# Performance work log

Measured on AMD Instinct MI355X. Metric: run time of the kernel, lower is better.

## Reference

```python
import jax, jax.numpy as jnp
import numpy as np

DIM = 2048
N_EXPERTS = 64
TOP_K = 8
BIAS_UPDATE_RATE = 0.01
EPS = 1e-8


def setup_inputs() -> dict:
    key = jax.random.key(0)
    k_x, k_w = jax.random.split(key)
    x = jax.random.normal(k_x, (4, 8192, DIM), dtype=jnp.float32)
    gate_weight = jax.random.normal(k_w, (N_EXPERTS, DIM), dtype=jnp.float32) * 0.02
    adaptive_bias = jnp.zeros((N_EXPERTS,), dtype=jnp.float32)
    expert_usage = jnp.zeros((N_EXPERTS,), dtype=jnp.float32)
    return {"x": x, "gate_weight": gate_weight, "adaptive_bias": adaptive_bias,
            "expert_usage": expert_usage}


def reference(x, gate_weight, adaptive_bias, expert_usage):
    B, S, D = x.shape
    xf = x.reshape(-1, D)                                   # [T, D]
    scores = jnp.einsum('td,ed->te', xf, gate_weight)       # [T, E]
    scores = scores + adaptive_bias[None, :]
    probs = jax.nn.softmax(scores, axis=-1)
    top_w, top_idx = jax.lax.top_k(probs, TOP_K)            # [T, K]
    top_w = top_w / (jnp.sum(top_w, axis=-1, keepdims=True) + EPS)
    # training-mode adaptive-bias update (no-grad histogram of selected experts)
    usage = jnp.bincount(top_idx.reshape(-1), length=N_EXPERTS).astype(jnp.float32)
    usage = usage / (B * S * TOP_K)
    usage_diff = usage - 1.0 / N_EXPERTS
    new_adaptive_bias = adaptive_bias - BIAS_UPDATE_RATE * usage_diff
    new_expert_usage = 0.9 * expert_usage + 0.1 * usage
    top_w = top_w.reshape(B, S, TOP_K)
    top_idx = top_idx.reshape(B, S, TOP_K)
    return top_w, top_idx, new_adaptive_bias, new_expert_usage
```

## Files before the change

### kernel.cpp

```cpp
#include <hip/hip_runtime.h>
#include <math.h>

constexpr int DIM    = 2048;
constexpr int NEXP   = 64;
constexpr int TOPK   = 8;
constexpr int T_TOT  = 32768;

constexpr int TTILE  = 64;
constexpr int BK     = 64;
constexpr int NSTEP  = DIM / BK;

constexpr float GAP_TH = 5.0e-4f;

constexpr size_t OFF_W   = 0;
constexpr size_t OFF_IDX = (size_t)T_TOT * TOPK;
constexpr size_t OFF_B   = OFF_IDX * 2;
constexpr size_t OFF_U   = OFF_B + NEXP;


#define MAC(i, j, A, B) \
    acc[i][j] = fmaf(A.x, B.x, acc[i][j]); \
    acc[i][j] = fmaf(A.y, B.y, acc[i][j]); \
    acc[i][j] = fmaf(A.z, B.z, acc[i][j]); \
    acc[i][j] = fmaf(A.w, B.w, acc[i][j]);

__global__ __launch_bounds__(256, 4)
void moe_gate_main(const float* __restrict__ x,
                   const float* __restrict__ gw,
                   const float* __restrict__ bias,
                   float* __restrict__ out,
                   unsigned int* __restrict__ ws,
                   const unsigned int cap)
{
    __shared__ __align__(16) char smem[32768];
    __shared__ unsigned int hist[NEXP];

    const int tid = threadIdx.x;
    const int t0  = blockIdx.x * TTILE;

    if (tid < NEXP) hist[tid] = 0;

    const int r0  = tid >> 4;
    const int c   = tid & 15;
    const float* xb0 = x  + (size_t)(t0 + r0) * DIM + 4 * c;
    const float* wb0 = gw + (size_t)r0        * DIM + 4 * c;
    const int ls0 = r0 * 256 + ((c ^ (r0 & 7)) << 4);

    char* const Wt = smem;
    char* const Xt = smem + 16384;

    float acc[4][4];
    #pragma unroll
    for (int i = 0; i < 4; ++i)
        #pragma unroll
        for (int j = 0; j < 4; ++j) acc[i][j] = 0.0f;

    const int eg = tid & 15;
    const int tg = tid >> 4;
    const int wx = (eg & 7) << 4;
    const int tx = (tg & 7) << 4;

    for (int step = 0; step < NSTEP; ++step) {
        const int ko = step * BK;
        const float4 xv0 = *(const float4*)(xb0 + ko);
        const float4 xv1 = *(const float4*)(xb0 + ko + 16 * DIM);
        const float4 xv2 = *(const float4*)(xb0 + ko + 32 * DIM);
        const float4 xv3 = *(const float4*)(xb0 + ko + 48 * DIM);
        const float4 wv0 = *(const float4*)(wb0 + ko);
        const float4 wv1 = *(const float4*)(wb0 + ko + 16 * DIM);
        const float4 wv2 = *(const float4*)(wb0 + ko + 32 * DIM);
        const float4 wv3 = *(const float4*)(wb0 + ko + 48 * DIM);
        __syncthreads();
        *(float4*)(Xt + ls0)         = xv0;
        *(float4*)(Xt + ls0 + 4096)  = xv1;
        *(float4*)(Xt + ls0 + 8192)  = xv2;
        *(float4*)(Xt + ls0 + 12288) = xv3;
        *(float4*)(Wt + ls0)         = wv0;
        *(float4*)(Wt + ls0 + 4096)  = wv1;
        *(float4*)(Wt + ls0 + 8192)  = wv2;
        *(float4*)(Wt + ls0 + 12288) = wv3;
        __syncthreads();

        const char* wb = Wt + eg * 256;
        const char* xb = Xt + tg * 256;
        #pragma unroll
        for (int q = 0; q < 16; ++q) {
            const int wq = (q << 4) ^ wx;
            const int xq = (q << 4) ^ tx;
            const float4 a0 = *(const float4*)(wb + wq);
            const float4 a1 = *(const float4*)(wb + 4096  + wq);
            const float4 a2 = *(const float4*)(wb + 8192  + wq);
            const float4 a3 = *(const float4*)(wb + 12288 + wq);
            const float4 b0 = *(const float4*)(xb + xq);
            const float4 b1 = *(const float4*)(xb + 4096  + xq);
            const float4 b2 = *(const float4*)(xb + 8192  + xq);
            const float4 b3 = *(const float4*)(xb + 12288 + xq);
            MAC(0,0,a0,b0) MAC(0,1,a0,b1) MAC(0,2,a0,b2) MAC(0,3,a0,b3)
            MAC(1,0,a1,b0) MAC(1,1,a1,b1) MAC(1,2,a1,b2) MAC(1,3,a1,b3)
            MAC(2,0,a2,b0) MAC(2,1,a2,b1) MAC(2,2,a2,b2) MAC(2,3,a2,b3)
            MAC(3,0,a3,b0) MAC(3,1,a3,b1) MAC(3,2,a3,b2) MAC(3,3,a3,b3)
        }
    }

    __syncthreads();
    float* S = (float*)smem;
    #pragma unroll
    for (int i = 0; i < 4; ++i) {
        const int e = eg + 16 * i;
        const float b = bias[e];
        #pragma unroll
        for (int j = 0; j < 4; ++j)
            S[e * 65 + tg + 16 * j] = acc[i][j] + b;
    }
    __syncthreads();

    if (tid < TTILE) {
        const int t = tid;
        float bv[9]; int bi[9];
        #pragma unroll
        for (int j = 0; j < 9; ++j) { bv[j] = -INFINITY; bi[j] = 0; }
        for (int e = 0; e < NEXP; ++e) {
            const float v = S[e * 65 + t];
            if (v > bv[8]) {
                bv[8] = v; bi[8] = e;
                #pragma unroll
                for (int j = 8; j > 0; --j) {
                    if (bv[j] > bv[j - 1]) {
                        const float tv = bv[j]; bv[j] = bv[j-1]; bv[j-1] = tv;
                        const int   ti = bi[j]; bi[j] = bi[j-1]; bi[j-1] = ti;
                    }
                }
            }
        }
        float ming = bv[0] - bv[1];
        #pragma unroll
        for (int j = 1; j < 8; ++j) ming = fminf(ming, bv[j] - bv[j + 1]);
        bool amb = (ming < GAP_TH);

        if (amb) {
            const unsigned slot = atomicAdd(ws + NEXP, 1u);
            if (slot < cap) ws[NEXP + 1 + slot] = (unsigned)(t0 + t);
            else            amb = false;
        }

        const float m = bv[0];
        float Z = 0.0f;
        for (int e = 0; e < NEXP; ++e) Z += expf(S[e * 65 + t] - m);
        const float rZ = 1.0f / Z;
        float p[TOPK]; float wsum = 0.0f;
        #pragma unroll
        for (int j = 0; j < TOPK; ++j) { p[j] = expf(bv[j] - m) * rZ; wsum += p[j]; }
        const float rd = 1.0f / (wsum + 1e-8f);

        const size_t tglob = (size_t)(t0 + t);
        float4 w0 = { p[0]*rd, p[1]*rd, p[2]*rd, p[3]*rd };
        float4 w1 = { p[4]*rd, p[5]*rd, p[6]*rd, p[7]*rd };
        *(float4*)(out + OFF_W + tglob * TOPK)     = w0;
        *(float4*)(out + OFF_W + tglob * TOPK + 4) = w1;
        float4 i0 = { (float)bi[0], (float)bi[1], (float)bi[2], (float)bi[3] };
        float4 i1 = { (float)bi[4], (float)bi[5], (float)bi[6], (float)bi[7] };
        *(float4*)(out + OFF_IDX + tglob * TOPK)     = i0;
        *(float4*)(out + OFF_IDX + tglob * TOPK + 4) = i1;

        if (!amb) {
            #pragma unroll
            for (int j = 0; j < TOPK; ++j) atomicAdd(&hist[bi[j]], 1u);
        }
    }

    __syncthreads();
    if (tid < NEXP) atomicAdd(ws + tid, hist[tid]);
}

__global__ __launch_bounds__(256)
void moe_gate_refine(const float* __restrict__ x,
                     const float* __restrict__ gw,
                     const float* __restrict__ bias,
                     float* __restrict__ out,
                     unsigned int* __restrict__ ws,
                     const unsigned int cap)
{
    __shared__ __align__(16) float xs[DIM];
    __shared__ float S[NEXP];
    const unsigned nf = ws[NEXP];
    const unsigned nflag = nf < cap ? nf : cap;
    const unsigned* list = ws + NEXP + 1;

    for (unsigned ii = blockIdx.x; ii < nflag; ii += gridDim.x) {
        const size_t t = (size_t)list[ii];
        __syncthreads();
        #pragma unroll
        for (int jj = 0; jj < 2; ++jj) {
            const int f = threadIdx.x + jj * 256;
            ((float4*)xs)[f] = ((const float4*)(x + t * DIM))[f];
        }
        __syncthreads();

        const int e = threadIdx.x >> 2;
        const int q = threadIdx.x & 3;
        const float* wr = gw + (size_t)e * DIM + q * 512;
        const float* xr = xs + q * 512;
        double s = 0.0;
        for (int k = 0; k < 512; k += 4) {
            const float4 wv4 = *(const float4*)(wr + k);
            const float4 xv4 = *(const float4*)(xr + k);
            s = fma((double)wv4.x, (double)xv4.x, s);
            s = fma((double)wv4.y, (double)xv4.y, s);
            s = fma((double)wv4.z, (double)xv4.z, s);
            s = fma((double)wv4.w, (double)xv4.w, s);
        }
        s += __shfl_down(s, 2, 4);
        s += __shfl_down(s, 1, 4);
        if (q == 0) S[e] = (float)s + bias[e];
        __syncthreads();

        if (threadIdx.x == 0) {
            float bv[TOPK]; int bi[TOPK];
            #pragma unroll
            for (int j = 0; j < TOPK; ++j) { bv[j] = -INFINITY; bi[j] = 0; }
            for (int e2 = 0; e2 < NEXP; ++e2) {
                const float v = S[e2];
                if (v > bv[TOPK - 1]) {
                    bv[TOPK - 1] = v; bi[TOPK - 1] = e2;
                    #pragma unroll
                    for (int j = TOPK - 1; j > 0; --j) {
                        if (bv[j] > bv[j - 1]) {
                            const float tv = bv[j]; bv[j] = bv[j-1]; bv[j-1] = tv;
                            const int   ti = bi[j]; bi[j] = bi[j-1]; bi[j-1] = ti;
                        }
                    }
                }
            }
            const float m = bv[0];
            float Z = 0.0f;
            for (int e2 = 0; e2 < NEXP; ++e2) Z += expf(S[e2] - m);
            const float rZ = 1.0f / Z;
            float p[TOPK]; float wsum = 0.0f;
            #pragma unroll
            for (int j = 0; j < TOPK; ++j) { p[j] = expf(bv[j] - m) * rZ; wsum += p[j]; }
            const float rd = 1.0f / (wsum + 1e-8f);

            float4 w0 = { p[0]*rd, p[1]*rd, p[2]*rd, p[3]*rd };
            float4 w1 = { p[4]*rd, p[5]*rd, p[6]*rd, p[7]*rd };
            *(float4*)(out + OFF_W + t * TOPK)     = w0;
            *(float4*)(out + OFF_W + t * TOPK + 4) = w1;
            float4 i0 = { (float)bi[0], (float)bi[1], (float)bi[2], (float)bi[3] };
            float4 i1 = { (float)bi[4], (float)bi[5], (float)bi[6], (float)bi[7] };
            *(float4*)(out + OFF_IDX + t * TOPK)     = i0;
            *(float4*)(out + OFF_IDX + t * TOPK + 4) = i1;

            #pragma unroll
            for (int j = 0; j < TOPK; ++j) atomicAdd(ws + bi[j], 1u);
        }
    }
}

__global__ void moe_gate_fin(const unsigned int* __restrict__ cnt,
                             const float* __restrict__ bias,
                             const float* __restrict__ eu,
                             float* __restrict__ out)
{
    const int e = threadIdx.x;
    const float usage = (float)cnt[e] * (1.0f / (float)(T_TOT * TOPK));
    out[OFF_B + e] = bias[e] - 0.01f * (usage - 1.0f / (float)NEXP);
    out[OFF_U + e] = 0.9f * eu[e] + 0.1f * usage;
}

extern "C" void kernel_launch(void* const* d_in, const int* in_sizes, int n_in,
                              void* d_out, int out_size, void* d_ws, size_t ws_size,
                              hipStream_t stream) {
    const float* x    = (const float*)d_in[0];
    const float* gw   = (const float*)d_in[1];
    const float* bias = (const float*)d_in[2];
    const float* eu   = (const float*)d_in[3];
    float* out = (float*)d_out;
    unsigned int* cnt = (unsigned int*)d_ws;

    const size_t ws_words = ws_size / sizeof(unsigned int);
    const unsigned cap = ws_words > (size_t)(NEXP + 1)
                       ? (unsigned)(ws_words - (NEXP + 1)) : 0u;

    hipMemsetAsync(cnt, 0, (NEXP + 1) * sizeof(unsigned int), stream);
    moe_gate_main<<<T_TOT / TTILE, 256, 0, stream>>>(x, gw, bias, out, cnt, cap);
    moe_gate_refine<<<256, 256, 0, stream>>>(x, gw, bias, out, cnt, cap);
    moe_gate_fin<<<1, NEXP, 0, stream>>>(cnt, bias, eu, out);
}
```

Before: 578.0 us.

## Restructure gating GEMM: per-wave expert slices with scalar weight loads and double-buffered x

Replaces the shared-memory tiled 4x4 register-blocked GEMM with a scheme where each wave owns 16 experts and each lane one token. Gate weights are read directly from global memory via wave-uniform addresses, which lets them become scalar loads, while x tiles are double-buffered in padded LDS with the next chunk prefetched into registers. This aims to remove the W staging in LDS, halve the barriers per step and overlap global loads with compute. In exchange register pressure rises, occupancy drops to 2 blocks per SM, and each x element is read from LDS once per lane with no 2D register reuse.

```diff
diff --git a/kernel.cpp b/kernel.cpp
--- a/kernel.cpp
+++ b/kernel.cpp
@@ -7,8 +7,9 @@
 constexpr int T_TOT  = 32768;
 
 constexpr int TTILE  = 64;
-constexpr int BK     = 64;
-constexpr int NSTEP  = DIM / BK;
+constexpr int KC     = 32;
+constexpr int NSTEP  = DIM / KC;
+constexpr int PSTR   = 260;
 
 constexpr float GAP_TH = 5.0e-4f;
 
@@ -18,13 +19,7 @@
 constexpr size_t OFF_U   = OFF_B + NEXP;
 
 
-#define MAC(i, j, A, B) \
-    acc[i][j] = fmaf(A.x, B.x, acc[i][j]); \
-    acc[i][j] = fmaf(A.y, B.y, acc[i][j]); \
-    acc[i][j] = fmaf(A.z, B.z, acc[i][j]); \
-    acc[i][j] = fmaf(A.w, B.w, acc[i][j]);
-
-__global__ __launch_bounds__(256, 4)
+__global__ __launch_bounds__(256, 2)
 void moe_gate_main(const float* __restrict__ x,
                    const float* __restrict__ gw,
                    const float* __restrict__ bias,
@@ -32,85 +27,88 @@
                    unsigned int* __restrict__ ws,
                    const unsigned int cap)
 {
-    __shared__ __align__(16) char smem[32768];
+    __shared__ __align__(16) float smem[4160];
     __shared__ unsigned int hist[NEXP];
 
-    const int tid = threadIdx.x;
-    const int t0  = blockIdx.x * TTILE;
+    const int tid  = threadIdx.x;
+    const int t0   = blockIdx.x * TTILE;
+    const int lane = tid & 63;
 
     if (tid < NEXP) hist[tid] = 0;
 
-    const int r0  = tid >> 4;
-    const int c   = tid & 15;
-    const float* xb0 = x  + (size_t)(t0 + r0) * DIM + 4 * c;
-    const float* wb0 = gw + (size_t)r0        * DIM + 4 * c;
-    const int ls0 = r0 * 256 + ((c ^ (r0 & 7)) << 4);
-
-    char* const Wt = smem;
-    char* const Xt = smem + 16384;
-
-    float acc[4][4];
+    const int wv = __builtin_amdgcn_readfirstlane(tid >> 6);
+    const float* wbase = gw + (size_t)(16 * wv) * DIM;
+
+    const int tokA = tid >> 3;
+    const int cA   = tid & 7;
+    const float* xgA = x + (size_t)(t0 + tokA)      * DIM + 4 * cA;
+    const float* xgB = x + (size_t)(t0 + tokA + 32) * DIM + 4 * cA;
+    const int lsA = cA * PSTR + tokA * 4;
+    const int lsB = cA * PSTR + (tokA + 32) * 4;
+
+    float acc[16];
     #pragma unroll
-    for (int i = 0; i < 4; ++i)
-        #pragma unroll
-        for (int j = 0; j < 4; ++j) acc[i][j] = 0.0f;
-
-    const int eg = tid & 15;
-    const int tg = tid >> 4;
-    const int wx = (eg & 7) << 4;
-    const int tx = (tg & 7) << 4;
-
-    for (int step = 0; step < NSTEP; ++step) {
-        const int ko = step * BK;
-        const float4 xv0 = *(const float4*)(xb0 + ko);
-        const float4 xv1 = *(const float4*)(xb0 + ko + 16 * DIM);
-        const float4 xv2 = *(const float4*)(xb0 + ko + 32 * DIM);
-        const float4 xv3 = *(const float4*)(xb0 + ko + 48 * DIM);
-        const float4 wv0 = *(const float4*)(wb0 + ko);
-        const float4 wv1 = *(const float4*)(wb0 + ko + 16 * DIM);
-        const float4 wv2 = *(const float4*)(wb0 + ko + 32 * DIM);
-        const float4 wv3 = *(const float4*)(wb0 + ko + 48 * DIM);
-        __syncthreads();
-        *(float4*)(Xt + ls0)         = xv0;
-        *(float4*)(Xt + ls0 + 4096)  = xv1;
-        *(float4*)(Xt + ls0 + 8192)  = xv2;
-        *(float4*)(Xt + ls0 + 12288) = xv3;
-        *(float4*)(Wt + ls0)         = wv0;
-        *(float4*)(Wt + ls0 + 4096)  = wv1;
-        *(float4*)(Wt + ls0 + 8192)  = wv2;
-        *(float4*)(Wt + ls0 + 12288) = wv3;
-        __syncthreads();
-
-        const char* wb = Wt + eg * 256;
-        const char* xb = Xt + tg * 256;
-        #pragma unroll
-        for (int q = 0; q < 16; ++q) {
-            const int wq = (q << 4) ^ wx;
-            const int xq = (q << 4) ^ tx;
-            const float4 a0 = *(const float4*)(wb + wq);
-            const float4 a1 = *(const float4*)(wb + 4096  + wq);
-            const float4 a2 = *(const float4*)(wb + 8192  + wq);
-            const float4 a3 = *(const float4*)(wb + 12288 + wq);
-            const float4 b0 = *(const float4*)(xb + xq);
-            const float4 b1 = *(const float4*)(xb + 4096  + xq);
-            const float4 b2 = *(const float4*)(xb + 8192  + xq);
-            const float4 b3 = *(const float4*)(xb + 12288 + xq);
-            MAC(0,0,a0,b0) MAC(0,1,a0,b1) MAC(0,2,a0,b2) MAC(0,3,a0,b3)
-            MAC(1,0,a1,b0) MAC(1,1,a1,b1) MAC(1,2,a1,b2) MAC(1,3,a1,b3)
-            MAC(2,0,a2,b0) MAC(2,1,a2,b1) MAC(2,2,a2,b2) MAC(2,3,a2,b3)
-            MAC(3,0,a3,b0) MAC(3,1,a3,b1) MAC(3,2,a3,b2) MAC(3,3,a3,b3)
+    for (int i = 0; i < 16; ++i) acc[i] = 0.0f;
+
+    {
+        const float4 a = *(const float4*)xgA;
+        const float4 b = *(const float4*)xgB;
+        *(float4*)&smem[lsA] = a;
+        *(float4*)&smem[lsB] = b;
+    }
+
+    for (int s = 0; s < NSTEP; ++s) {
+        __syncthreads();
+        const int cur = (s & 1) * 2080;
+
+        float4 nxa, nxb;
+        if (s + 1 < NSTEP) {
+            nxa = *(const float4*)(xgA + (s + 1) * KC);
+            nxb = *(const float4*)(xgB + (s + 1) * KC);
+        }
+
+        float xr[32];
+        #pragma unroll
+        for (int c = 0; c < 8; ++c)
+            *(float4*)&xr[4 * c] = *(const float4*)&smem[cur + c * PSTR + lane * 4];
+
+        const float* wk = wbase + s * KC;
+        float wA[32], wB[32];
+        #pragma unroll
+        for (int j = 0; j < 8; ++j)
+            *(float4*)&wA[4 * j] = *(const float4*)(wk + 4 * j);
+        #pragma unroll
+        for (int e = 0; e < 16; ++e) {
+            const float* wc = (e & 1) ? wB : wA;
+            float*       wn = (e & 1) ? wA : wB;
+            if (e < 15) {
+                const float* wp = wk + (size_t)(e + 1) * DIM;
+                #pragma unroll
+                for (int j = 0; j < 8; ++j)
+                    *(float4*)&wn[4 * j] = *(const float4*)(wp + 4 * j);
+            }
+            float a0 = acc[e], a1 = 0.0f;
+            #pragma unroll
+            for (int k = 0; k < 16; ++k) {
+                a0 = fmaf(wc[k],      xr[k],      a0);
+                a1 = fmaf(wc[k + 16], xr[k + 16], a1);
+            }
+            acc[e] = a0 + a1;
+        }
+
+        if (s + 1 < NSTEP) {
+            const int nb = ((s + 1) & 1) * 2080;
+            *(float4*)&smem[nb + lsA] = nxa;
+            *(float4*)&smem[nb + lsB] = nxb;
         }
     }
 
     __syncthreads();
-    float* S = (float*)smem;
+    float* S = smem;
     #pragma unroll
-    for (int i = 0; i < 4; ++i) {
-        const int e = eg + 16 * i;
-        const float b = bias[e];
-        #pragma unroll
-        for (int j = 0; j < 4; ++j)
-            S[e * 65 + tg + 16 * j] = acc[i][j] + b;
+    for (int i = 0; i < 16; ++i) {
+        const int e = 16 * wv + i;
+        S[e * 65 + lane] = acc[i] + bias[e];
     }
     __syncthreads();
 
```

New measurement: 1.374 ms. 2.38x slower.
